# Kernel optimization log

Measured on AMD Instinct MI355X. Metric: run time of the kernel, lower is better.

Reference implementation:

```python
import jax, jax.numpy as jnp
import numpy as np

ND_WEIGHT = 1.0
NUM_CLASS = 1000
B, D = 16384, 2048


def setup_inputs() -> dict:
    key = jax.random.key(0)
    k1, k2, k3, k4 = jax.random.split(key, 4)
    s_emb = jax.random.normal(k1, (B, D), dtype=jnp.float32)
    t_emb = jax.random.normal(k2, (B, D), dtype=jnp.float32)
    T_EMB = jax.random.normal(k3, (NUM_CLASS, D), dtype=jnp.float32)
    labels = jax.random.randint(k4, (B,), 0, NUM_CLASS, dtype=jnp.int64)
    return {"s_emb": s_emb, "t_emb": t_emb, "T_EMB": T_EMB, "labels": labels}


def reference(s_emb, t_emb, T_EMB, labels):
    # Gather per-sample class centers: [B, D]
    centers = T_EMB[labels]
    # Unit-normalize each center (L2 along feature dim)
    e_c = centers / jnp.linalg.norm(centers, axis=-1, keepdims=True)
    # Per-sample max of student/teacher embedding norms: [B]
    s_norm = jnp.linalg.norm(s_emb, axis=-1)
    t_norm = jnp.linalg.norm(t_emb, axis=-1)
    max_norm = jnp.maximum(s_norm, t_norm)
    # 1 - <s, e_c> / max_norm, summed then averaged, scaled by nd_weight
    dots = jnp.sum(s_emb * e_c, axis=-1)
    loss_sum = jnp.sum(1.0 - dots / max_norm)
    return loss_sum * ND_WEIGHT / s_emb.shape[0]
```

## Files before the change

### kernel.cpp

```cpp
#include <hip/hip_runtime.h>


#define NROWS  16384
#define DDIM   2048
#define BLK    256
#define WPB    (BLK / 64)
#define GRID   (NROWS / WPB)

typedef float v4f __attribute__((ext_vector_type(4)));

__global__ __launch_bounds__(BLK, 2) void dnl_main_kernel(
    const float* __restrict__ s_emb,
    const float* __restrict__ t_emb,
    const float* __restrict__ T_EMB,
    const int*   __restrict__ labels,
    float*       __restrict__ partial)
{
    const int tid  = threadIdx.x;
    const int lane = tid & 63;
    const int row  = blockIdx.x * WPB + (tid >> 6);

    const int label = labels[row];

    const v4f* s4 = (const v4f*)(s_emb + (size_t)row   * DDIM);
    const v4f* t4 = (const v4f*)(t_emb + (size_t)row   * DDIM);
    const v4f* c4 = (const v4f*)(T_EMB + (size_t)label * DDIM);

    float ss = 0.f, tt = 0.f, sc = 0.f, cc = 0.f;
    #pragma unroll
    for (int j = 0; j < 8; ++j) {
        const int k = lane + j * 64;
        const v4f s = __builtin_nontemporal_load(&s4[k]);
        const v4f t = __builtin_nontemporal_load(&t4[k]);
        const v4f c = c4[k];
        ss += s.x*s.x + s.y*s.y + s.z*s.z + s.w*s.w;
        tt += t.x*t.x + t.y*t.y + t.z*t.z + t.w*t.w;
        sc += s.x*c.x + s.y*c.y + s.z*c.z + s.w*c.w;
        cc += c.x*c.x + c.y*c.y + c.z*c.z + c.w*c.w;
    }

    #pragma unroll
    for (int off = 32; off > 0; off >>= 1) {
        ss += __shfl_xor(ss, off, 64);
        tt += __shfl_xor(tt, off, 64);
        sc += __shfl_xor(sc, off, 64);
        cc += __shfl_xor(cc, off, 64);
    }

    if (lane == 0) {
        const float max_norm = fmaxf(sqrtf(ss), sqrtf(tt));
        partial[row] = 1.0f - sc / (sqrtf(cc) * max_norm);
    }
}

__global__ __launch_bounds__(BLK) void dnl_reduce_kernel(
    const float* __restrict__ partial,
    float*       __restrict__ out)
{
    const int tid = threadIdx.x;
    const float4* p4 = (const float4*)partial;
    float sum = 0.f;
    #pragma unroll
    for (int j = 0; j < 16; ++j) {
        const float4 v = p4[tid + j * BLK];
        sum += v.x + v.y + v.z + v.w;
    }

    #pragma unroll
    for (int off = 32; off > 0; off >>= 1)
        sum += __shfl_xor(sum, off, 64);

    __shared__ float red[4];
    if ((tid & 63) == 0) red[tid >> 6] = sum;
    __syncthreads();
    if (tid == 0)
        out[0] = (red[0] + red[1] + red[2] + red[3]) * (1.0f / (float)NROWS);
}

__global__ __launch_bounds__(BLK, 2) void dnl_main_atomic_kernel(
    const float* __restrict__ s_emb,
    const float* __restrict__ t_emb,
    const float* __restrict__ T_EMB,
    const int*   __restrict__ labels,
    float*       __restrict__ out)
{
    const int tid  = threadIdx.x;
    const int lane = tid & 63;
    const int row  = blockIdx.x * WPB + (tid >> 6);
    const int label = labels[row];

    const v4f* s4 = (const v4f*)(s_emb + (size_t)row   * DDIM);
    const v4f* t4 = (const v4f*)(t_emb + (size_t)row   * DDIM);
    const v4f* c4 = (const v4f*)(T_EMB + (size_t)label * DDIM);

    float ss = 0.f, tt = 0.f, sc = 0.f, cc = 0.f;
    #pragma unroll
    for (int j = 0; j < 8; ++j) {
        const int k = lane + j * 64;
        const v4f s = __builtin_nontemporal_load(&s4[k]);
        const v4f t = __builtin_nontemporal_load(&t4[k]);
        const v4f c = c4[k];
        ss += s.x*s.x + s.y*s.y + s.z*s.z + s.w*s.w;
        tt += t.x*t.x + t.y*t.y + t.z*t.z + t.w*t.w;
        sc += s.x*c.x + s.y*c.y + s.z*c.z + s.w*c.w;
        cc += c.x*c.x + c.y*c.y + c.z*c.z + c.w*c.w;
    }
    #pragma unroll
    for (int off = 32; off > 0; off >>= 1) {
        ss += __shfl_xor(ss, off, 64);
        tt += __shfl_xor(tt, off, 64);
        sc += __shfl_xor(sc, off, 64);
        cc += __shfl_xor(cc, off, 64);
    }
    if (lane == 0) {
        const float max_norm = fmaxf(sqrtf(ss), sqrtf(tt));
        atomicAdd(out, (1.0f - sc / (sqrtf(cc) * max_norm)) * (1.0f / (float)NROWS));
    }
}

extern "C" void kernel_launch(void* const* d_in, const int* in_sizes, int n_in,
                              void* d_out, int out_size, void* d_ws, size_t ws_size,
                              hipStream_t stream) {
    const float* s_emb  = (const float*)d_in[0];
    const float* t_emb  = (const float*)d_in[1];
    const float* T_EMB  = (const float*)d_in[2];
    const int*   labels = (const int*)d_in[3];
    float* out = (float*)d_out;

    if (ws_size >= (size_t)NROWS * sizeof(float)) {
        float* partial = (float*)d_ws;
        dnl_main_kernel<<<GRID, BLK, 0, stream>>>(s_emb, t_emb, T_EMB, labels, partial);
        dnl_reduce_kernel<<<1, BLK, 0, stream>>>(partial, out);
    } else {
        hipMemsetAsync(d_out, 0, sizeof(float), stream);
        dnl_main_atomic_kernel<<<GRID, BLK, 0, stream>>>(s_emb, t_emb, T_EMB, labels, out);
    }
}
```

Before: 265.2 us.

## Process four rows per wave with double-buffered register prefetch

Each wave now handles four rows, issuing the loads for the next row into a second register buffer before reducing the current one, to keep more memory requests in flight per wave. Nontemporal load hints are dropped in favour of plain loads, and launch bounds are relaxed to allow higher register use. The trade is fewer blocks and lower occupancy in exchange for more per-wave memory-level parallelism. The atomic fallback path keeps one row per wave with its own grid size.

Result: slower. 281.8 us (+6.3%).

```diff
diff --git a/kernel.cpp b/kernel.cpp
--- a/kernel.cpp
+++ b/kernel.cpp
@@ -5,11 +5,17 @@
 #define DDIM   2048
 #define BLK    256
 #define WPB    (BLK / 64)
-#define GRID   (NROWS / WPB)
+#define RPW    4
+#define GRID   (NROWS / (WPB * RPW))
+#define GRID_AT (NROWS / WPB)
 
 typedef float v4f __attribute__((ext_vector_type(4)));
 
-__global__ __launch_bounds__(BLK, 2) void dnl_main_kernel(
+__device__ __forceinline__ float dot4(const v4f a, const v4f b) {
+    return a.x*b.x + a.y*b.y + a.z*b.z + a.w*b.w;
+}
+
+__global__ __launch_bounds__(BLK, 1) void dnl_main_kernel(
     const float* __restrict__ s_emb,
     const float* __restrict__ t_emb,
     const float* __restrict__ T_EMB,
@@ -18,39 +24,56 @@
 {
     const int tid  = threadIdx.x;
     const int lane = tid & 63;
-    const int row  = blockIdx.x * WPB + (tid >> 6);
+    const int wave = blockIdx.x * WPB + (tid >> 6);
+    const int row0 = wave * RPW;
 
-    const int label = labels[row];
+    v4f sA[8], tA[8], cA[8];
+    v4f sB[8], tB[8], cB[8];
 
-    const v4f* s4 = (const v4f*)(s_emb + (size_t)row   * DDIM);
-    const v4f* t4 = (const v4f*)(t_emb + (size_t)row   * DDIM);
-    const v4f* c4 = (const v4f*)(T_EMB + (size_t)label * DDIM);
+    auto issue = [&](int row, v4f* S, v4f* T, v4f* C) {
+        const int label = labels[row];
+        const v4f* s4 = (const v4f*)(s_emb + (size_t)row   * DDIM);
+        const v4f* t4 = (const v4f*)(t_emb + (size_t)row   * DDIM);
+        const v4f* c4 = (const v4f*)(T_EMB + (size_t)label * DDIM);
+        #pragma unroll
+        for (int j = 0; j < 8; ++j) {
+            const int k = lane + j * 64;
+            S[j] = s4[k];
+            T[j] = t4[k];
+            C[j] = c4[k];
+        }
+    };
 
-    float ss = 0.f, tt = 0.f, sc = 0.f, cc = 0.f;
-    #pragma unroll
-    for (int j = 0; j < 8; ++j) {
-        const int k = lane + j * 64;
-        const v4f s = __builtin_nontemporal_load(&s4[k]);
-        const v4f t = __builtin_nontemporal_load(&t4[k]);
-        const v4f c = c4[k];
-        ss += s.x*s.x + s.y*s.y + s.z*s.z + s.w*s.w;
-        tt += t.x*t.x + t.y*t.y + t.z*t.z + t.w*t.w;
-        sc += s.x*c.x + s.y*c.y + s.z*c.z + s.w*c.w;
-        cc += c.x*c.x + c.y*c.y + c.z*c.z + c.w*c.w;
-    }
+    auto consume = [&](int row, const v4f* S, const v4f* T, const v4f* C) {
+        float ss = 0.f, tt = 0.f, sc = 0.f, cc = 0.f;
+        #pragma unroll
+        for (int j = 0; j < 8; ++j) {
+            ss += dot4(S[j], S[j]);
+            tt += dot4(T[j], T[j]);
+            sc += dot4(S[j], C[j]);
+            cc += dot4(C[j], C[j]);
+        }
+        #pragma unroll
+        for (int off = 32; off > 0; off >>= 1) {
+            ss += __shfl_xor(ss, off, 64);
+            tt += __shfl_xor(tt, off, 64);
+            sc += __shfl_xor(sc, off, 64);
+            cc += __shfl_xor(cc, off, 64);
+        }
+        if (lane == 0) {
+            const float max_norm = fmaxf(sqrtf(ss), sqrtf(tt));
+            partial[row] = 1.0f - sc / (sqrtf(cc) * max_norm);
+        }
+    };
 
-    #pragma unroll
-    for (int off = 32; off > 0; off >>= 1) {
-        ss += __shfl_xor(ss, off, 64);
-        tt += __shfl_xor(tt, off, 64);
-        sc += __shfl_xor(sc, off, 64);
-        cc += __shfl_xor(cc, off, 64);
-    }
-
-    if (lane == 0) {
-        const float max_norm = fmaxf(sqrtf(ss), sqrtf(tt));
-        partial[row] = 1.0f - sc / (sqrtf(cc) * max_norm);
-    }
+    issue  (row0 + 0, sA, tA, cA);
+    issue  (row0 + 1, sB, tB, cB);
+    consume(row0 + 0, sA, tA, cA);
+    issue  (row0 + 2, sA, tA, cA);
+    consume(row0 + 1, sB, tB, cB);
+    issue  (row0 + 3, sB, tB, cB);
+    consume(row0 + 2, sA, tA, cA);
+    consume(row0 + 3, sB, tB, cB);
 }
 
 __global__ __launch_bounds__(BLK) void dnl_reduce_kernel(
@@ -97,13 +120,13 @@
     #pragma unroll
     for (int j = 0; j < 8; ++j) {
         const int k = lane + j * 64;
-        const v4f s = __builtin_nontemporal_load(&s4[k]);
-        const v4f t = __builtin_nontemporal_load(&t4[k]);
+        const v4f s = s4[k];
+        const v4f t = t4[k];
         const v4f c = c4[k];
-        ss += s.x*s.x + s.y*s.y + s.z*s.z + s.w*s.w;
-        tt += t.x*t.x + t.y*t.y + t.z*t.z + t.w*t.w;
-        sc += s.x*c.x + s.y*c.y + s.z*c.z + s.w*c.w;
-        cc += c.x*c.x + c.y*c.y + c.z*c.z + c.w*c.w;
+        ss += dot4(s, s);
+        tt += dot4(t, t);
+        sc += dot4(s, c);
+        cc += dot4(c, c);
     }
     #pragma unroll
     for (int off = 32; off > 0; off >>= 1) {
@@ -133,6 +156,6 @@
         dnl_reduce_kernel<<<1, BLK, 0, stream>>>(partial, out);
     } else {
         hipMemsetAsync(d_out, 0, sizeof(float), stream);
-        dnl_main_atomic_kernel<<<GRID, BLK, 0, stream>>>(s_emb, t_emb, T_EMB, labels, out);
+        dnl_main_atomic_kernel<<<GRID_AT, BLK, 0, stream>>>(s_emb, t_emb, T_EMB, labels, out);
     }
 }
```
